# Kernel tuning notes

Measured on AMD Instinct MI355X. Metric: run time of the kernel, lower is better.

The kernel has to match this reference:

```python
import jax, jax.numpy as jnp
import numpy as np

N_NODES = 100000
N_EDGES = 1200000
IN_FEATS = 64
OUT_FEATS = 32
K_HOPS = 4  # k = len([in_feats] + hidden_lst) with hidden_lst=[64,64,32]


def setup_inputs() -> dict:
    key = jax.random.key(0)
    k1, k2, k3, k4, k5 = jax.random.split(key, 5)
    features = jax.random.normal(k1, (N_NODES, IN_FEATS), dtype=jnp.float32)
    src = jax.random.randint(k2, (N_EDGES,), 0, N_NODES, dtype=jnp.int64)
    dst = jax.random.randint(k3, (N_EDGES,), 0, N_NODES, dtype=jnp.int64)
    # fc layer of SGConv: Linear(in_feats -> out_feats) with bias
    bound = 1.0 / np.sqrt(IN_FEATS)
    W = jax.random.uniform(k4, (OUT_FEATS, IN_FEATS), dtype=jnp.float32,
                           minval=-bound, maxval=bound)
    b = jax.random.uniform(k5, (OUT_FEATS,), dtype=jnp.float32,
                           minval=-bound, maxval=bound)
    return {"features": features, "src": src, "dst": dst, "W": W, "b": b}


def reference(features, src, dst, W, b):
    # DGL SGConv with norm='both': symmetric normalization each hop.
    # in-degree of each dst node, clamped to >= 1
    deg = jax.ops.segment_sum(jnp.ones((N_EDGES,), dtype=features.dtype),
                              dst, num_segments=N_NODES)
    norm = jnp.clip(deg, 1.0, None) ** -0.5  # [N]
    norm = norm[:, None]                      # [N, 1]
    h = features
    for _ in range(K_HOPS):
        h = h * norm                                            # D^{-1/2} x
        h = jax.ops.segment_sum(h[src], dst, num_segments=N_NODES)  # A x (SpMM)
        h = h * norm                                            # D^{-1/2}
    # final linear layer
    return h @ W.T + b
```

## Files before the change

### kernel.cpp

```cpp
#include <hip/hip_runtime.h>
#include <hip/hip_fp16.h>
#include <cstdint>

#define NNODES 100000
#define NEDGES 1200000
#define INF 64
#define OUTF 32
#define SCAN_B 256
#define NBUCK ((NNODES + SCAN_B - 1) / SCAN_B)
#define PCAP 4608
#define BIN_EPT 16
#define BIN_THREADS (NEDGES / BIN_EPT)
#define BIN_BLOCKS ((BIN_THREADS + 255) / 256)
#define PROJ_NPB 16
#define PROJ_BLOCKS (NNODES / PROJ_NPB)
#define CUR_PAD 16
#define WST 66

__global__ __launch_bounds__(256) void k_initcur(int* __restrict__ gcur) {
    int i = blockIdx.x * 256 + threadIdx.x;
    if (i < NBUCK) gcur[i * CUR_PAD] = i * PCAP;
}

__global__ __launch_bounds__(256) void k_binproj(const int4* __restrict__ src4,
                                                 const int4* __restrict__ dst4,
                                                 int* __restrict__ gcur,
                                                 unsigned* __restrict__ packed,
                                                 const float4* __restrict__ feat4,
                                                 const float4* __restrict__ W4,
                                                 __half2* __restrict__ h0_p) {
    __shared__ __align__(16) char smem[12672];
    int tid = threadIdx.x;
    if (blockIdx.x < BIN_BLOCKS) {
        int* cnt = (int*)smem;
        int* base = cnt + NBUCK;
        for (int i = tid; i < NBUCK; i += 256) cnt[i] = 0;
        __syncthreads();
        int gid = blockIdx.x * 256 + tid;
        bool act = gid < BIN_THREADS;
        int4 s4[4], d4[4];
        if (act) {
#pragma unroll
            for (int k = 0; k < 4; ++k) {
                s4[k] = src4[(size_t)gid * 4 + k];
                d4[k] = dst4[(size_t)gid * 4 + k];
                atomicAdd(&cnt[d4[k].x >> 8], 1);
                atomicAdd(&cnt[d4[k].y >> 8], 1);
                atomicAdd(&cnt[d4[k].z >> 8], 1);
                atomicAdd(&cnt[d4[k].w >> 8], 1);
            }
        }
        __syncthreads();
        for (int i = tid; i < NBUCK; i += 256) {
            int c = cnt[i];
            base[i] = c ? atomicAdd(&gcur[i * CUR_PAD], c) : 0;
            cnt[i] = 0;
        }
        __syncthreads();
        if (act) {
#pragma unroll
            for (int k = 0; k < 4; ++k) {
                int ss[4] = {s4[k].x, s4[k].y, s4[k].z, s4[k].w};
                int dd[4] = {d4[k].x, d4[k].y, d4[k].z, d4[k].w};
#pragma unroll
                for (int j = 0; j < 4; ++j) {
                    int b = dd[j] >> 8;
                    int rel = atomicAdd(&cnt[b], 1);
                    packed[base[b] + rel] =
                        ((unsigned)(dd[j] & 255) << 17) | (unsigned)ss[j];
                }
            }
        }
    } else {
        float (*Ws)[WST] = (float (*)[WST])smem;
        float (*Fs)[WST] = (float (*)[WST])(smem + 32 * WST * 4);
        int node0 = (blockIdx.x - BIN_BLOCKS) * PROJ_NPB;
        for (int i = tid; i < 512; i += 256) {
            float4 w = W4[i];
            int f = i * 4, of = f >> 6, k = f & 63;
            Ws[of][k] = w.x; Ws[of][k + 1] = w.y;
            Ws[of][k + 2] = w.z; Ws[of][k + 3] = w.w;
        }
        {
            int n = node0 + (tid >> 4), q = tid & 15;
            float4 v = feat4[(size_t)n * 16 + q];
            int c = q * 4;
            Fs[tid >> 4][c] = v.x; Fs[tid >> 4][c + 1] = v.y;
            Fs[tid >> 4][c + 2] = v.z; Fs[tid >> 4][c + 3] = v.w;
        }
        __syncthreads();
        int ln = tid >> 4, n = node0 + ln;
        int of0 = (tid & 15) * 2;
        const float2* fp = (const float2*)&Fs[ln][0];
        const float2* w0 = (const float2*)&Ws[of0][0];
        const float2* w1 = (const float2*)&Ws[of0 + 1][0];
        float a0 = 0.0f, a1 = 0.0f;
#pragma unroll
        for (int k2 = 0; k2 < 32; ++k2) {
            float2 f = fp[k2], x = w0[k2], y = w1[k2];
            a0 += f.x * x.x + f.y * x.y;
            a1 += f.x * y.x + f.y * y.y;
        }
        h0_p[(size_t)n * 16 + (tid & 15)] = __floats2half2_rn(a0, a1);
    }
}

__global__ __launch_bounds__(256) void k_place(const unsigned* __restrict__ packed,
                                               const int* __restrict__ gcur,
                                               int* __restrict__ col,
                                               unsigned* __restrict__ rowsd,
                                               float* __restrict__ norm) {
    __shared__ unsigned sin_[PCAP];
    __shared__ int stage[PCAP];
    __shared__ int deg[SCAN_B];
    __shared__ int rs[SCAN_B];
    int b = blockIdx.x, tid = threadIdx.x;
    int node0 = b * SCAN_B;
    int nn = (NNODES - node0 < SCAN_B) ? (NNODES - node0) : SCAN_B;
    int ebase = b * PCAP;
    int nedge = gcur[b * CUR_PAD] - ebase;
    deg[tid] = 0;
    __syncthreads();
    for (int i = tid; i < nedge; i += 256) {
        unsigned pk = packed[ebase + i];
        sin_[i] = pk;
        atomicAdd(&deg[pk >> 17], 1);
    }
    __syncthreads();
    int d = deg[tid];
    rs[tid] = d;
    __syncthreads();
    for (int st = 1; st < SCAN_B; st <<= 1) {
        int add = (tid >= st) ? rs[tid - st] : 0;
        __syncthreads();
        rs[tid] += add;
        __syncthreads();
    }
    int myoff = rs[tid] - d;
    if (tid < nn) {
        norm[node0 + tid] = rsqrtf(d < 1 ? 1.0f : (float)d);
        rowsd[node0 + tid] = ((unsigned)(ebase + myoff) << 11) | (unsigned)d;
    }
    deg[tid] = myoff;
    __syncthreads();
    for (int i = tid; i < nedge; i += 256) {
        unsigned pk = sin_[i];
        int rel = atomicAdd(&deg[pk >> 17], 1);
        stage[rel] = (int)(pk & 0x1FFFFu);
    }
    __syncthreads();
    for (int i = tid; i < nedge; i += 256) col[ebase + i] = stage[i];
}

__global__ __launch_bounds__(256) void k_scale(uint4* __restrict__ h0,
                                               const float* __restrict__ norm) {
    int i = blockIdx.x * 256 + threadIdx.x;
    if (i >= NNODES * 4) return;
    float nn = norm[i >> 2];
    uint4 r = h0[i];
    float2 f0 = __half22float2(*(const __half2*)&r.x);
    float2 f1 = __half22float2(*(const __half2*)&r.y);
    float2 f2 = __half22float2(*(const __half2*)&r.z);
    float2 f3 = __half22float2(*(const __half2*)&r.w);
    *(__half2*)&r.x = __floats2half2_rn(nn * f0.x, nn * f0.y);
    *(__half2*)&r.y = __floats2half2_rn(nn * f1.x, nn * f1.y);
    *(__half2*)&r.z = __floats2half2_rn(nn * f2.x, nn * f2.y);
    *(__half2*)&r.w = __floats2half2_rn(nn * f3.x, nn * f3.y);
    h0[i] = r;
}

template <bool LAST>
__global__ __launch_bounds__(256) void k_gather(const uint4* __restrict__ uin,
                                                void* __restrict__ uout,
                                                const unsigned* __restrict__ rowsd,
                                                const int* __restrict__ col,
                                                const float* __restrict__ norm,
                                                const float4* __restrict__ bias4) {
    int t = blockIdx.x * 256 + threadIdx.x;
    int node = t >> 2;
    if (node >= NNODES) return;
    int lane = t & 3;
    unsigned rd = rowsd[node];
    int e = rd >> 11;
    int re = e + (int)(rd & 2047u);
    const uint4* up = uin + lane;
    float4 accA = make_float4(0.f, 0.f, 0.f, 0.f);
    float4 accB = make_float4(0.f, 0.f, 0.f, 0.f);
    auto add = [&](uint4 r) {
        float2 f0 = __half22float2(*(const __half2*)&r.x);
        float2 f1 = __half22float2(*(const __half2*)&r.y);
        float2 f2 = __half22float2(*(const __half2*)&r.z);
        float2 f3 = __half22float2(*(const __half2*)&r.w);
        accA.x += f0.x; accA.y += f0.y; accA.z += f1.x; accA.w += f1.y;
        accB.x += f2.x; accB.y += f2.y; accB.z += f3.x; accB.w += f3.y;
    };
    for (; e + 7 < re; e += 8) {
        int s0 = col[e],     s1 = col[e + 1], s2 = col[e + 2], s3 = col[e + 3];
        int s4 = col[e + 4], s5 = col[e + 5], s6 = col[e + 6], s7 = col[e + 7];
        uint4 r0 = up[(size_t)s0 * 4];
        uint4 r1 = up[(size_t)s1 * 4];
        uint4 r2 = up[(size_t)s2 * 4];
        uint4 r3 = up[(size_t)s3 * 4];
        uint4 r4 = up[(size_t)s4 * 4];
        uint4 r5 = up[(size_t)s5 * 4];
        uint4 r6 = up[(size_t)s6 * 4];
        uint4 r7 = up[(size_t)s7 * 4];
        add(r0); add(r1); add(r2); add(r3);
        add(r4); add(r5); add(r6); add(r7);
    }
    for (; e < re; ++e) add(up[(size_t)col[e] * 4]);
    float nn = norm[node];
    float w = LAST ? nn : nn * nn;
    accA.x *= w; accA.y *= w; accA.z *= w; accA.w *= w;
    accB.x *= w; accB.y *= w; accB.z *= w; accB.w *= w;
    if (LAST) {
        float4 b0 = bias4[lane * 2], b1 = bias4[lane * 2 + 1];
        accA.x += b0.x; accA.y += b0.y; accA.z += b0.z; accA.w += b0.w;
        accB.x += b1.x; accB.y += b1.y; accB.z += b1.z; accB.w += b1.w;
        float4* o = (float4*)uout;
        o[(size_t)node * 8 + lane * 2]     = accA;
        o[(size_t)node * 8 + lane * 2 + 1] = accB;
    } else {
        uint4 r;
        *(__half2*)&r.x = __floats2half2_rn(accA.x, accA.y);
        *(__half2*)&r.y = __floats2half2_rn(accA.z, accA.w);
        *(__half2*)&r.z = __floats2half2_rn(accB.x, accB.y);
        *(__half2*)&r.w = __floats2half2_rn(accB.z, accB.w);
        ((uint4*)uout)[(size_t)node * 4 + lane] = r;
    }
}

extern "C" void kernel_launch(void* const* d_in, const int* in_sizes, int n_in,
                              void* d_out, int out_size, void* d_ws, size_t ws_size,
                              hipStream_t stream) {
    const float* feat = (const float*)d_in[0];
    const int*   src  = (const int*)d_in[1];
    const int*   dst  = (const int*)d_in[2];
    const float* W    = (const float*)d_in[3];
    const float* b    = (const float*)d_in[4];
    float* out = (float*)d_out;

    char* ws = (char*)d_ws;
    size_t off = 0;
    auto alloc = [&](size_t bytes) {
        void* p = ws + off;
        off = (off + bytes + 255) & ~(size_t)255;
        return p;
    };
    float*    norm   = (float*)alloc((size_t)NNODES * 4);
    unsigned* rowsd  = (unsigned*)alloc((size_t)NNODES * 4);
    int*      gcur   = (int*)alloc((size_t)NBUCK * CUR_PAD * 4);
    unsigned* packed = (unsigned*)alloc((size_t)NBUCK * PCAP * 4);
    int*      col    = (int*)alloc((size_t)NBUCK * PCAP * 4);
    void*     h0     = alloc((size_t)NNODES * OUTF * 2);
    void*     h1     = alloc((size_t)NNODES * OUTF * 2);

    k_initcur<<<(NBUCK + 255) / 256, 256, 0, stream>>>(gcur);
    k_binproj<<<BIN_BLOCKS + PROJ_BLOCKS, 256, 0, stream>>>(
        (const int4*)src, (const int4*)dst, gcur, packed,
        (const float4*)feat, (const float4*)W, (__half2*)h0);
    k_place<<<NBUCK, 256, 0, stream>>>(packed, gcur, col, rowsd, norm);

    const int sgrid = (NNODES * 4 + 255) / 256;
    k_scale<<<sgrid, 256, 0, stream>>>((uint4*)h0, norm);

    k_gather<false><<<sgrid, 256, 0, stream>>>(
        (const uint4*)h0, h1, rowsd, col, norm, nullptr);
    k_gather<false><<<sgrid, 256, 0, stream>>>(
        (const uint4*)h1, h0, rowsd, col, norm, nullptr);
    k_gather<false><<<sgrid, 256, 0, stream>>>(
        (const uint4*)h0, h1, rowsd, col, norm, nullptr);
    k_gather<true><<<sgrid, 256, 0, stream>>>(
        (const uint4*)h1, out, rowsd, col, norm, (const float4*)b);
}
```

Before: 140.6 us.

## Pad CSR rows to multiples of eight with a zero sentinel and fuse scaling into placement

Each node's adjacency row is padded to a multiple of 8 entries, with padding pointing at an extra zero row appended to the feature buffers. This lets the gather kernel load column indices as int4 vectors and drop its scalar tail loop. The separate D^{-1/2} scaling kernel is folded into k_place, which saves one launch and one pass over h0. In exchange, the padded edges add extra gathers of the sentinel row and more column storage, and the PADCAP bucket capacity is fixed.

```diff
diff --git a/kernel.cpp b/kernel.cpp
--- a/kernel.cpp
+++ b/kernel.cpp
@@ -9,6 +9,7 @@
 #define SCAN_B 256
 #define NBUCK ((NNODES + SCAN_B - 1) / SCAN_B)
 #define PCAP 4608
+#define PADCAP 5632
 #define BIN_EPT 16
 #define BIN_THREADS (NEDGES / BIN_EPT)
 #define BIN_BLOCKS ((BIN_THREADS + 255) / 256)
@@ -17,9 +18,13 @@
 #define CUR_PAD 16
 #define WST 66
 
-__global__ __launch_bounds__(256) void k_initcur(int* __restrict__ gcur) {
+__global__ __launch_bounds__(256) void k_initcur(int* __restrict__ gcur,
+                                                 uint4* __restrict__ h0,
+                                                 uint4* __restrict__ h1) {
     int i = blockIdx.x * 256 + threadIdx.x;
     if (i < NBUCK) gcur[i * CUR_PAD] = i * PCAP;
+    if (i >= 256 && i < 260) h0[(size_t)NNODES * 4 + (i - 256)] = make_uint4(0, 0, 0, 0);
+    if (i >= 260 && i < 264) h1[(size_t)NNODES * 4 + (i - 260)] = make_uint4(0, 0, 0, 0);
 }
 
 __global__ __launch_bounds__(256) void k_binproj(const int4* __restrict__ src4,
@@ -109,15 +114,19 @@
                                                const int* __restrict__ gcur,
                                                int* __restrict__ col,
                                                unsigned* __restrict__ rowsd,
-                                               float* __restrict__ norm) {
+                                               float* __restrict__ norm,
+                                               uint4* __restrict__ h0) {
     __shared__ unsigned sin_[PCAP];
-    __shared__ int stage[PCAP];
+    __shared__ int stage[PADCAP];
     __shared__ int deg[SCAN_B];
     __shared__ int rs[SCAN_B];
+    __shared__ int cur[SCAN_B];
+    __shared__ int tot;
     int b = blockIdx.x, tid = threadIdx.x;
     int node0 = b * SCAN_B;
     int nn = (NNODES - node0 < SCAN_B) ? (NNODES - node0) : SCAN_B;
     int ebase = b * PCAP;
+    int pbase = b * PADCAP;
     int nedge = gcur[b * CUR_PAD] - ebase;
     deg[tid] = 0;
     __syncthreads();
@@ -128,7 +137,8 @@
     }
     __syncthreads();
     int d = deg[tid];
-    rs[tid] = d;
+    int dpad = (d + 7) & ~7;
+    rs[tid] = dpad;
     __syncthreads();
     for (int st = 1; st < SCAN_B; st <<= 1) {
         int add = (tid >= st) ? rs[tid - st] : 0;
@@ -136,44 +146,48 @@
         rs[tid] += add;
         __syncthreads();
     }
-    int myoff = rs[tid] - d;
+    int myoff = rs[tid] - dpad;
+    if (tid == SCAN_B - 1) tot = rs[tid];
+    float mynorm = rsqrtf(d < 1 ? 1.0f : (float)d);
     if (tid < nn) {
-        norm[node0 + tid] = rsqrtf(d < 1 ? 1.0f : (float)d);
-        rowsd[node0 + tid] = ((unsigned)(ebase + myoff) << 11) | (unsigned)d;
-    }
-    deg[tid] = myoff;
+        norm[node0 + tid] = mynorm;
+        rowsd[node0 + tid] =
+            ((unsigned)((pbase + myoff) >> 3) << 9) | (unsigned)(dpad >> 3);
+    }
+    cur[tid] = myoff;
+    __syncthreads();
+    for (int i = tid; i < tot; i += 256) stage[i] = NNODES;
     __syncthreads();
     for (int i = tid; i < nedge; i += 256) {
         unsigned pk = sin_[i];
-        int rel = atomicAdd(&deg[pk >> 17], 1);
+        int rel = atomicAdd(&cur[pk >> 17], 1);
         stage[rel] = (int)(pk & 0x1FFFFu);
     }
     __syncthreads();
-    for (int i = tid; i < nedge; i += 256) col[ebase + i] = stage[i];
-}
-
-__global__ __launch_bounds__(256) void k_scale(uint4* __restrict__ h0,
-                                               const float* __restrict__ norm) {
-    int i = blockIdx.x * 256 + threadIdx.x;
-    if (i >= NNODES * 4) return;
-    float nn = norm[i >> 2];
-    uint4 r = h0[i];
-    float2 f0 = __half22float2(*(const __half2*)&r.x);
-    float2 f1 = __half22float2(*(const __half2*)&r.y);
-    float2 f2 = __half22float2(*(const __half2*)&r.z);
-    float2 f3 = __half22float2(*(const __half2*)&r.w);
-    *(__half2*)&r.x = __floats2half2_rn(nn * f0.x, nn * f0.y);
-    *(__half2*)&r.y = __floats2half2_rn(nn * f1.x, nn * f1.y);
-    *(__half2*)&r.z = __floats2half2_rn(nn * f2.x, nn * f2.y);
-    *(__half2*)&r.w = __floats2half2_rn(nn * f3.x, nn * f3.y);
-    h0[i] = r;
+    for (int i = tid; i < tot; i += 256) col[pbase + i] = stage[i];
+    if (tid < nn) {
+        uint4* hp = h0 + (size_t)(node0 + tid) * 4;
+#pragma unroll
+        for (int k = 0; k < 4; ++k) {
+            uint4 r = hp[k];
+            float2 f0 = __half22float2(*(const __half2*)&r.x);
+            float2 f1 = __half22float2(*(const __half2*)&r.y);
+            float2 f2 = __half22float2(*(const __half2*)&r.z);
+            float2 f3 = __half22float2(*(const __half2*)&r.w);
+            *(__half2*)&r.x = __floats2half2_rn(mynorm * f0.x, mynorm * f0.y);
+            *(__half2*)&r.y = __floats2half2_rn(mynorm * f1.x, mynorm * f1.y);
+            *(__half2*)&r.z = __floats2half2_rn(mynorm * f2.x, mynorm * f2.y);
+            *(__half2*)&r.w = __floats2half2_rn(mynorm * f3.x, mynorm * f3.y);
+            hp[k] = r;
+        }
+    }
 }
 
 template <bool LAST>
 __global__ __launch_bounds__(256) void k_gather(const uint4* __restrict__ uin,
                                                 void* __restrict__ uout,
                                                 const unsigned* __restrict__ rowsd,
-                                                const int* __restrict__ col,
+                                                const int4* __restrict__ colv,
                                                 const float* __restrict__ norm,
                                                 const float4* __restrict__ bias4) {
     int t = blockIdx.x * 256 + threadIdx.x;
@@ -181,8 +195,8 @@
     if (node >= NNODES) return;
     int lane = t & 3;
     unsigned rd = rowsd[node];
-    int e = rd >> 11;
-    int re = e + (int)(rd & 2047u);
+    int c4 = (int)(rd >> 9) * 2;
+    int n8 = (int)(rd & 511u);
     const uint4* up = uin + lane;
     float4 accA = make_float4(0.f, 0.f, 0.f, 0.f);
     float4 accB = make_float4(0.f, 0.f, 0.f, 0.f);
@@ -194,21 +208,20 @@
         accA.x += f0.x; accA.y += f0.y; accA.z += f1.x; accA.w += f1.y;
         accB.x += f2.x; accB.y += f2.y; accB.z += f3.x; accB.w += f3.y;
     };
-    for (; e + 7 < re; e += 8) {
-        int s0 = col[e],     s1 = col[e + 1], s2 = col[e + 2], s3 = col[e + 3];
-        int s4 = col[e + 4], s5 = col[e + 5], s6 = col[e + 6], s7 = col[e + 7];
-        uint4 r0 = up[(size_t)s0 * 4];
-        uint4 r1 = up[(size_t)s1 * 4];
-        uint4 r2 = up[(size_t)s2 * 4];
-        uint4 r3 = up[(size_t)s3 * 4];
-        uint4 r4 = up[(size_t)s4 * 4];
-        uint4 r5 = up[(size_t)s5 * 4];
-        uint4 r6 = up[(size_t)s6 * 4];
-        uint4 r7 = up[(size_t)s7 * 4];
+    for (int j = 0; j < n8; ++j) {
+        int4 c0 = colv[c4 + j * 2];
+        int4 c1 = colv[c4 + j * 2 + 1];
+        uint4 r0 = up[(size_t)c0.x * 4];
+        uint4 r1 = up[(size_t)c0.y * 4];
+        uint4 r2 = up[(size_t)c0.z * 4];
+        uint4 r3 = up[(size_t)c0.w * 4];
+        uint4 r4 = up[(size_t)c1.x * 4];
+        uint4 r5 = up[(size_t)c1.y * 4];
+        uint4 r6 = up[(size_t)c1.z * 4];
+        uint4 r7 = up[(size_t)c1.w * 4];
         add(r0); add(r1); add(r2); add(r3);
         add(r4); add(r5); add(r6); add(r7);
     }
-    for (; e < re; ++e) add(up[(size_t)col[e] * 4]);
     float nn = norm[node];
     float w = LAST ? nn : nn * nn;
     accA.x *= w; accA.y *= w; accA.z *= w; accA.w *= w;
@@ -251,25 +264,24 @@
     unsigned* rowsd  = (unsigned*)alloc((size_t)NNODES * 4);
     int*      gcur   = (int*)alloc((size_t)NBUCK * CUR_PAD * 4);
     unsigned* packed = (unsigned*)alloc((size_t)NBUCK * PCAP * 4);
-    int*      col    = (int*)alloc((size_t)NBUCK * PCAP * 4);
-    void*     h0     = alloc((size_t)NNODES * OUTF * 2);
-    void*     h1     = alloc((size_t)NNODES * OUTF * 2);
-
-    k_initcur<<<(NBUCK + 255) / 256, 256, 0, stream>>>(gcur);
+    int*      col    = (int*)alloc((size_t)NBUCK * PADCAP * 4);
+    void*     h0     = alloc((size_t)(NNODES + 1) * OUTF * 2);
+    void*     h1     = alloc((size_t)(NNODES + 1) * OUTF * 2);
+
+    k_initcur<<<2, 256, 0, stream>>>(gcur, (uint4*)h0, (uint4*)h1);
     k_binproj<<<BIN_BLOCKS + PROJ_BLOCKS, 256, 0, stream>>>(
         (const int4*)src, (const int4*)dst, gcur, packed,
         (const float4*)feat, (const float4*)W, (__half2*)h0);
-    k_place<<<NBUCK, 256, 0, stream>>>(packed, gcur, col, rowsd, norm);
-
-    const int sgrid = (NNODES * 4 + 255) / 256;
-    k_scale<<<sgrid, 256, 0, stream>>>((uint4*)h0, norm);
-
-    k_gather<false><<<sgrid, 256, 0, stream>>>(
-        (const uint4*)h0, h1, rowsd, col, norm, nullptr);
-    k_gather<false><<<sgrid, 256, 0, stream>>>(
-        (const uint4*)h1, h0, rowsd, col, norm, nullptr);
-    k_gather<false><<<sgrid, 256, 0, stream>>>(
-        (const uint4*)h0, h1, rowsd, col, norm, nullptr);
-    k_gather<true><<<sgrid, 256, 0, stream>>>(
-        (const uint4*)h1, out, rowsd, col, norm, (const float4*)b);
-}
+    k_place<<<NBUCK, 256, 0, stream>>>(packed, gcur, col, rowsd, norm,
+                                       (uint4*)h0);
+
+    const int ggrid = (NNODES * 4 + 255) / 256;
+    k_gather<false><<<ggrid, 256, 0, stream>>>(
+        (const uint4*)h0, h1, rowsd, (const int4*)col, norm, nullptr);
+    k_gather<false><<<ggrid, 256, 0, stream>>>(
+        (const uint4*)h1, h0, rowsd, (const int4*)col, norm, nullptr);
+    k_gather<false><<<ggrid, 256, 0, stream>>>(
+        (const uint4*)h0, h1, rowsd, (const int4*)col, norm, nullptr);
+    k_gather<true><<<ggrid, 256, 0, stream>>>(
+        (const uint4*)h1, out, rowsd, (const int4*)col, norm, (const float4*)b);
+}
```

Result: faster. 119.6 us (-15.0%).
